# Performance work log

Measured on AMD Instinct MI355X. Metric: run time of the kernel, lower is better.

The kernel has to match this reference:

```python
import jax, jax.numpy as jnp
import numpy as np

N, H, R, C = 50000, 16, 32, 8   # nodes, hidden, relations, classes
E = 1600000                      # edges (avg degree 32)


def setup_inputs() -> dict:
    key = jax.random.key(0)
    ks = jax.random.split(key, 6)
    edge_index = jax.random.randint(ks[0], (2, E), 0, N)
    edge_type = jax.random.randint(ks[1], (E,), 0, R)
    w1 = jax.random.normal(ks[2], (R, N, H), dtype=jnp.float32) * 0.05
    root1 = jax.random.normal(ks[3], (N, H), dtype=jnp.float32) * 0.05
    b1 = jnp.zeros((H,), jnp.float32)
    w2 = jax.random.normal(ks[4], (R, H, C), dtype=jnp.float32) * 0.05
    root2 = jax.random.normal(ks[5], (H, C), dtype=jnp.float32) * 0.05
    b2 = jnp.zeros((C,), jnp.float32)
    return {"edge_index": edge_index, "edge_type": edge_type,
            "w1": w1, "root1": root1, "b1": b1,
            "w2": w2, "root2": root2, "b2": b2}


def _rel_mean_agg(msgs, dst, edge_type, num_nodes, num_rel):
    """PyG RGCNConv aggregation: mean over edges within each (relation, target)
    pair, then sum over relations. msgs: [E, d] -> [num_nodes, d]."""
    seg = edge_type * num_nodes + dst                      # combined segment id
    tot = num_rel * num_nodes
    summed = jax.ops.segment_sum(msgs, seg, num_segments=tot)      # [R*N, d]
    cnt = jax.ops.segment_sum(jnp.ones((msgs.shape[0],), msgs.dtype), seg,
                              num_segments=tot)                    # [R*N]
    mean = summed / jnp.maximum(cnt, 1.0)[:, None]
    return mean.reshape(num_rel, num_nodes, -1).sum(axis=0)       # [N, d]


def reference(edge_index, edge_type, w1, root1, b1, w2, root2, b2):
    src, dst = edge_index[0], edge_index[1]
    # ---- layer 1: x = None -> message is weight row indexed by (rel, src)
    msgs1 = w1[edge_type, src]                             # [E, H] gather
    x = _rel_mean_agg(msgs1, dst, edge_type, N, R) + root1 + b1
    x = jax.nn.relu(x)
    # ---- layer 2: precompute per-relation transforms once: [R, N, C]
    xw = jnp.einsum('nh,rhc->rnc', x, w2)
    msgs2 = xw[edge_type, src]                             # [E, C] gather
    out = _rel_mean_agg(msgs2, dst, edge_type, N, R) + x @ root2 + b2
    return jax.nn.log_softmax(out, axis=1)
```

## Files before the change

### kernel.cpp

```cpp
#include <hip/hip_runtime.h>
#include <hip/hip_bf16.h>


constexpr int Nn = 50000;
constexpr int Hh = 16;
constexpr int Rr = 32;
constexpr int Cc = 8;
constexpr int Ee = 1600000;
constexpr int CHUNK = 4096;
constexpr int NC = (Ee + CHUNK - 1) / CHUNK;
constexpr int DSH = 7;
constexpr unsigned DLOWM = 127u;
constexpr int NBKT = (Nn + 127) / 128;
constexpr int K1 = (NC + 255) / 256;
constexpr int K2 = (NBKT + 255) / 256;

__device__ __forceinline__ float b2f(__hip_bfloat16 v) { return __bfloat162float(v); }
__device__ __forceinline__ float bs2f(unsigned short u) {
    return __uint_as_float(((unsigned)u) << 16);
}

__global__ __launch_bounds__(256) void histA_kernel(const int* __restrict__ dst,
                                                    unsigned* __restrict__ H,
                                                    const unsigned short* __restrict__ w1s,
                                                    int* __restrict__ flag) {
    __shared__ unsigned hb[NBKT];
    int c = blockIdx.x, tid = threadIdx.x;
    if (c == 0 && tid == 0) {
        int hits = 0;
        for (int i = 0; i < 64; ++i) {
            unsigned short u = w1s[2 * i];
            int e = (u >> 7) & 0xFF;
            if (e >= 100 && e <= 130) ++hits;
        }
        *flag = (hits >= 32) ? 1 : 0;
    }
    for (int i = tid; i < NBKT; i += 256) hb[i] = 0;
    __syncthreads();
    int base = c * CHUNK;
    int n = min(CHUNK, Ee - base);
    for (int i = tid; i < n; i += 256)
        atomicAdd(&hb[((unsigned)dst[base + i]) >> DSH], 1u);
    __syncthreads();
    for (int i = tid; i < NBKT; i += 256) H[(size_t)c * NBKT + i] = hb[i];
}

__global__ __launch_bounds__(256) void scanB1_kernel(unsigned* __restrict__ H,
                                                     unsigned* __restrict__ bt) {
    __shared__ int lsum[4];
    int b = blockIdx.x, t = threadIdx.x, lane = t & 63, wv = t >> 6;
    int c0 = t * K1;
    int v[K1];
#pragma unroll
    for (int j = 0; j < K1; ++j) {
        int c = c0 + j;
        v[j] = (c < NC) ? (int)H[(size_t)c * NBKT + b] : 0;
    }
    int tot = 0;
#pragma unroll
    for (int j = 0; j < K1; ++j) { int tmp = v[j]; v[j] = tot; tot += tmp; }
    int s = tot;
#pragma unroll
    for (int o = 1; o < 64; o <<= 1) { int u = __shfl_up(s, o, 64); if (lane >= o) s += u; }
    if (lane == 63) lsum[wv] = s;
    __syncthreads();
    int basev = 0;
    for (int j = 0; j < wv; ++j) basev += lsum[j];
    int excl = basev + s - tot;
#pragma unroll
    for (int j = 0; j < K1; ++j) {
        int c = c0 + j;
        if (c < NC) H[(size_t)c * NBKT + b] = (unsigned)(excl + v[j]);
    }
    if (t == 255) bt[b] = (unsigned)(basev + s);
}

__global__ __launch_bounds__(256) void scanB2_kernel(const unsigned* __restrict__ bt,
                                                     unsigned* __restrict__ rbase) {
    __shared__ int lsum[4];
    int t = threadIdx.x, lane = t & 63, wv = t >> 6;
    int c0 = t * K2;
    int v[K2];
#pragma unroll
    for (int j = 0; j < K2; ++j) {
        int c = c0 + j;
        v[j] = (c < NBKT) ? (int)bt[c] : 0;
    }
    int tot = 0;
#pragma unroll
    for (int j = 0; j < K2; ++j) { int tmp = v[j]; v[j] = tot; tot += tmp; }
    int s = tot;
#pragma unroll
    for (int o = 1; o < 64; o <<= 1) { int u = __shfl_up(s, o, 64); if (lane >= o) s += u; }
    if (lane == 63) lsum[wv] = s;
    __syncthreads();
    int basev = 0;
    for (int j = 0; j < wv; ++j) basev += lsum[j];
    int excl = basev + s - tot;
#pragma unroll
    for (int j = 0; j < K2; ++j) {
        int c = c0 + j;
        if (c < NBKT) rbase[c] = (unsigned)(excl + v[j]);
    }
    if (t == 255) rbase[NBKT] = (unsigned)(basev + s);
}

__global__ __launch_bounds__(256) void scatC_kernel(const int* __restrict__ src,
                                                    const int* __restrict__ dst,
                                                    const int* __restrict__ et,
                                                    const unsigned* __restrict__ H,
                                                    const unsigned* __restrict__ rbase,
                                                    unsigned* __restrict__ rec) {
    __shared__ unsigned bb[NBKT];
    __shared__ unsigned hb[NBKT];
    int c = blockIdx.x, tid = threadIdx.x;
    for (int i = tid; i < NBKT; i += 256) {
        bb[i] = H[(size_t)c * NBKT + i] + rbase[i];
        hb[i] = 0;
    }
    __syncthreads();
    int base = c * CHUNK;
    int n = min(CHUNK, Ee - base);
    for (int i = tid; i < n; i += 256) {
        int e = base + i;
        unsigned d = (unsigned)dst[e];
        unsigned r = (unsigned)et[e];
        unsigned sv = (unsigned)src[e];
        unsigned bkt = d >> DSH;
        unsigned rank = atomicAdd(&hb[bkt], 1u);
        rec[bb[bkt] + rank] = sv | (r << 16) | ((d & DLOWM) << 21);
    }
}

__global__ __launch_bounds__(256) void sortD_kernel(const unsigned* __restrict__ rec,
                                                    const unsigned* __restrict__ rbase,
                                                    unsigned* __restrict__ sorted,
                                                    int* __restrict__ offs) {
    __shared__ unsigned cnt[128 * 33];
    __shared__ unsigned sb[128 * 33];
    __shared__ int l2s[2];
    int b = blockIdx.x, t = threadIdx.x, lane = t & 63, wv = t >> 6;
    for (int i = t; i < 128 * 33; i += 256) { cnt[i] = 0; sb[i] = 0; }
    __syncthreads();
    unsigned rb = rbase[b], re = rbase[b + 1];
    int n = (int)(re - rb);
    for (int i = t; i < n; i += 256) {
        unsigned w = rec[rb + i];
        atomicAdd(&cnt[((w >> 21) & 127u) * 33 + ((w >> 16) & 31u)], 1u);
    }
    __syncthreads();
    int deg = 0;
    if (t < 128) {
#pragma unroll
        for (int r = 0; r < 32; ++r) {
            unsigned cc = cnt[t * 33 + r];
            sb[t * 33 + r] = (unsigned)deg;
            deg += (int)cc;
        }
    }
    int s = deg;
#pragma unroll
    for (int o = 1; o < 64; o <<= 1) { int u = __shfl_up(s, o, 64); if (lane >= o) s += u; }
    if (lane == 63 && wv < 2) l2s[wv] = s;
    __syncthreads();
    if (t < 128) {
        int excl = s - deg + (wv == 1 ? l2s[0] : 0);
        unsigned ab = rb + (unsigned)excl;
        int d = b * 128 + t;
        if (d <= Nn) offs[d] = (int)ab;
#pragma unroll
        for (int r = 0; r < 32; ++r) sb[t * 33 + r] += ab;
    }
    __syncthreads();
    for (int i = t; i < n; i += 256) {
        unsigned w = rec[rb + i];
        unsigned dlow = (w >> 21) & 127u, rel = (w >> 16) & 31u, sv = w & 0xFFFFu;
        int cell = (int)dlow * 33 + (int)rel;
        unsigned pos = atomicAdd(&sb[cell], 1u);
        unsigned cc = cnt[cell];
        if (cc > 2047u) cc = 2047u;
        sorted[pos] = sv | (rel << 16) | (cc << 21);
    }
}

__global__ __launch_bounds__(256) void l1_kernel(const unsigned* __restrict__ sorted,
                                                 const int* __restrict__ offs,
                                                 const void* __restrict__ w1,
                                                 const void* __restrict__ root1,
                                                 const void* __restrict__ b1,
                                                 const int* __restrict__ flag,
                                                 float* __restrict__ x) {
    int tid = threadIdx.x, w = tid >> 6, lane = tid & 63;
    int ep = lane >> 2, hp = lane & 3;
    int isbf = *flag;
    int d = blockIdx.x * 4 + w;
    int off = offs[d], deg = offs[d + 1] - off;
    float a0 = 0.f, a1 = 0.f, a2 = 0.f, a3 = 0.f;
    if (isbf) {
#pragma unroll 2
        for (int i = ep; i < deg; i += 16) {
            unsigned p = sorted[off + i];
            int cnt = p >> 21, rel = (p >> 16) & 31, s = p & 0xFFFF;
            float inv = __builtin_amdgcn_rcpf((float)cnt);
            ushort4 v = ((const ushort4*)w1)[((size_t)rel * Nn + s) * 4 + hp];
            a0 += inv * bs2f(v.x); a1 += inv * bs2f(v.y);
            a2 += inv * bs2f(v.z); a3 += inv * bs2f(v.w);
        }
    } else {
#pragma unroll 2
        for (int i = ep; i < deg; i += 16) {
            unsigned p = sorted[off + i];
            int cnt = p >> 21, rel = (p >> 16) & 31, s = p & 0xFFFF;
            float inv = __builtin_amdgcn_rcpf((float)cnt);
            float4 v = ((const float4*)w1)[((size_t)rel * Nn + s) * 4 + hp];
            a0 += inv * v.x; a1 += inv * v.y; a2 += inv * v.z; a3 += inv * v.w;
        }
    }
#pragma unroll
    for (int o = 4; o < 64; o <<= 1) {
        a0 += __shfl_xor(a0, o, 64);
        a1 += __shfl_xor(a1, o, 64);
        a2 += __shfl_xor(a2, o, 64);
        a3 += __shfl_xor(a3, o, 64);
    }
    if (ep == 0) {
        float r0, r1, r2, r3, bb0, bb1, bb2, bb3;
        if (isbf) {
            ushort4 rv = ((const ushort4*)root1)[(size_t)d * 4 + hp];
            ushort4 bv = ((const ushort4*)b1)[hp];
            r0 = bs2f(rv.x); r1 = bs2f(rv.y); r2 = bs2f(rv.z); r3 = bs2f(rv.w);
            bb0 = bs2f(bv.x); bb1 = bs2f(bv.y); bb2 = bs2f(bv.z); bb3 = bs2f(bv.w);
        } else {
            float4 rv = ((const float4*)root1)[(size_t)d * 4 + hp];
            float4 bv = ((const float4*)b1)[hp];
            r0 = rv.x; r1 = rv.y; r2 = rv.z; r3 = rv.w;
            bb0 = bv.x; bb1 = bv.y; bb2 = bv.z; bb3 = bv.w;
        }
        float v0 = a0 + r0 + bb0, v1 = a1 + r1 + bb1;
        float v2 = a2 + r2 + bb2, v3 = a3 + r3 + bb3;
        *(float4*)(x + (size_t)d * Hh + hp * 4) =
            make_float4(v0 > 0.f ? v0 : 0.f, v1 > 0.f ? v1 : 0.f,
                        v2 > 0.f ? v2 : 0.f, v3 > 0.f ? v3 : 0.f);
    }
}

__global__ __launch_bounds__(256) void l2_kernel(const unsigned* __restrict__ sorted,
                                                 const int* __restrict__ offs,
                                                 const float* __restrict__ x,
                                                 const void* __restrict__ w2,
                                                 const void* __restrict__ root2,
                                                 const void* __restrict__ b2v,
                                                 const int* __restrict__ flag,
                                                 void* __restrict__ out) {
    __shared__ float w2s[32 * 132];
    __shared__ float rsh[128];
    __shared__ float b2sh[8];
    int tid = threadIdx.x, w = tid >> 6, lane = tid & 63;
    int isbf = *flag;
    {
        int r = tid >> 3, cc = tid & 7;
        if (isbf) {
            const __hip_bfloat16* W = (const __hip_bfloat16*)w2 + r * 128 + cc;
#pragma unroll
            for (int h = 0; h < 16; ++h) w2s[r * 132 + cc * 16 + h] = b2f(W[h * 8]);
        } else {
            const float* W = (const float*)w2 + r * 128 + cc;
#pragma unroll
            for (int h = 0; h < 16; ++h) w2s[r * 132 + cc * 16 + h] = W[h * 8];
        }
    }
    if (tid < 128) rsh[tid] = isbf ? b2f(((const __hip_bfloat16*)root2)[tid])
                                   : ((const float*)root2)[tid];
    if (tid < 8)   b2sh[tid] = isbf ? b2f(((const __hip_bfloat16*)b2v)[tid])
                                    : ((const float*)b2v)[tid];
    __syncthreads();
    int ep = lane >> 3, c = lane & 7;
    int d = blockIdx.x * 4 + w;
    int off = offs[d], deg = offs[d + 1] - off;
    float acc = 0.0f;
    for (int i0 = 0; i0 < deg; i0 += 8) {
        int i = i0 + ep;
        if (i < deg) {
            unsigned p = sorted[off + i];
            int cnt = p >> 21, rel = (p >> 16) & 31, s = p & 0xFFFF;
            float inv = __builtin_amdgcn_rcpf((float)cnt);
            const float4* xr = (const float4*)(x + (size_t)s * Hh);
            float4 x0 = xr[0], x1 = xr[1], x2 = xr[2], x3 = xr[3];
            const float4* wv = (const float4*)(w2s + rel * 132 + c * 16);
            float4 w0 = wv[0], w1v = wv[1], w2v = wv[2], w3 = wv[3];
            float dot = x0.x*w0.x + x0.y*w0.y + x0.z*w0.z + x0.w*w0.w
                      + x1.x*w1v.x + x1.y*w1v.y + x1.z*w1v.z + x1.w*w1v.w
                      + x2.x*w2v.x + x2.y*w2v.y + x2.z*w2v.z + x2.w*w2v.w
                      + x3.x*w3.x + x3.y*w3.y + x3.z*w3.z + x3.w*w3.w;
            acc += inv * dot;
        }
    }
    acc += __shfl_xor(acc, 8, 64);
    acc += __shfl_xor(acc, 16, 64);
    acc += __shfl_xor(acc, 32, 64);
    if (ep == 0) {
        const float4* xr = (const float4*)(x + (size_t)d * Hh);
        float4 x0 = xr[0], x1 = xr[1], x2 = xr[2], x3 = xr[3];
        float xv[16] = {x0.x,x0.y,x0.z,x0.w, x1.x,x1.y,x1.z,x1.w,
                        x2.x,x2.y,x2.z,x2.w, x3.x,x3.y,x3.z,x3.w};
        float v = acc + b2sh[c];
#pragma unroll
        for (int h = 0; h < 16; ++h) v += xv[h] * rsh[h * 8 + c];
        float m = v;
#pragma unroll
        for (int o = 1; o < 8; o <<= 1) m = fmaxf(m, __shfl_xor(m, o, 8));
        float ssum = __expf(v - m);
#pragma unroll
        for (int o = 1; o < 8; o <<= 1) ssum += __shfl_xor(ssum, o, 8);
        float res = v - m - __logf(ssum);
        if (isbf) ((__hip_bfloat16*)out)[(size_t)d * Cc + c] = __float2bfloat16(res);
        else      ((float*)out)[(size_t)d * Cc + c] = res;
    }
}

extern "C" void kernel_launch(void* const* d_in, const int* in_sizes, int n_in,
                              void* d_out, int out_size, void* d_ws, size_t ws_size,
                              hipStream_t stream) {
    const int* edge_index = (const int*)d_in[0];
    const int* src = edge_index;
    const int* dst = edge_index + Ee;
    const int* et  = (const int*)d_in[1];
    const void* w1    = d_in[2];
    const void* root1 = d_in[3];
    const void* b1    = d_in[4];
    const void* w2    = d_in[5];
    const void* root2 = d_in[6];
    const void* b2    = d_in[7];

    unsigned* rec    = (unsigned*)d_ws;
    unsigned* sorted = rec + Ee;
    unsigned* H      = sorted + Ee;
    unsigned* bt     = H + (size_t)NC * NBKT;
    unsigned* rbase  = bt + NBKT;
    int* offs        = (int*)(rbase + NBKT + 1);
    int* flag        = offs + Nn + 4;
    float* x         = (float*)rec;

    histA_kernel<<<NC, 256, 0, stream>>>(dst, H, (const unsigned short*)w1, flag);
    scanB1_kernel<<<NBKT, 256, 0, stream>>>(H, bt);
    scanB2_kernel<<<1, 256, 0, stream>>>(bt, rbase);
    scatC_kernel<<<NC, 256, 0, stream>>>(src, dst, et, H, rbase, rec);
    sortD_kernel<<<NBKT, 256, 0, stream>>>(rec, rbase, sorted, offs);
    l1_kernel<<<Nn / 4, 256, 0, stream>>>(sorted, offs, w1, root1, b1, flag, x);
    l2_kernel<<<Nn / 4, 256, 0, stream>>>(sorted, offs, x, w2, root2, b2, flag, d_out);
}
```

Measured before the change: 299.3 us.

## Replace histogram/scan/scatter pipeline with atomic fixed-stride bucket scatter

The separate histogram, two-level scan and scatter kernels are merged into one scatter kernel. Each block counts its edges per destination bucket in shared memory, then reserves space with global atomics into buckets of a fixed stride (5120 slots per 128 nodes), so no global prefix sum is needed. Buckets are no longer contiguous, so the sort kernel stores a per-node 16-bit degree for l1/l2 instead of differencing offsets. Both rebuilt kernels now use 512 threads. This removes two launches and a pass over dst plus the per-chunk histogram matrix, but it depends on no bucket exceeding the fixed capacity, which holds for the uniform random graph but not in general.

```diff
diff --git a/kernel.cpp b/kernel.cpp
--- a/kernel.cpp
+++ b/kernel.cpp
@@ -4,7 +4,6 @@
 
 constexpr int Nn = 50000;
 constexpr int Hh = 16;
-constexpr int Rr = 32;
 constexpr int Cc = 8;
 constexpr int Ee = 1600000;
 constexpr int CHUNK = 4096;
@@ -12,21 +11,25 @@
 constexpr int DSH = 7;
 constexpr unsigned DLOWM = 127u;
 constexpr int NBKT = (Nn + 127) / 128;
-constexpr int K1 = (NC + 255) / 256;
-constexpr int K2 = (NBKT + 255) / 256;
+constexpr int STRIDE = 5120;
 
 __device__ __forceinline__ float b2f(__hip_bfloat16 v) { return __bfloat162float(v); }
 __device__ __forceinline__ float bs2f(unsigned short u) {
     return __uint_as_float(((unsigned)u) << 16);
 }
 
-__global__ __launch_bounds__(256) void histA_kernel(const int* __restrict__ dst,
-                                                    unsigned* __restrict__ H,
-                                                    const unsigned short* __restrict__ w1s,
-                                                    int* __restrict__ flag) {
+__global__ __launch_bounds__(512) void scat_kernel(const int* __restrict__ src,
+                                                   const int* __restrict__ dst,
+                                                   const int* __restrict__ et,
+                                                   unsigned* __restrict__ gcnt,
+                                                   unsigned* __restrict__ rec,
+                                                   const unsigned short* __restrict__ w1s,
+                                                   int* __restrict__ flag) {
     __shared__ unsigned hb[NBKT];
-    int c = blockIdx.x, tid = threadIdx.x;
-    if (c == 0 && tid == 0) {
+    __shared__ unsigned bb[NBKT];
+    __shared__ unsigned rk[NBKT];
+    int c = blockIdx.x, t = threadIdx.x;
+    if (c == 0 && t == 0) {
         int hits = 0;
         for (int i = 0; i < 64; ++i) {
             unsigned short u = w1s[2 * i];
@@ -35,116 +38,44 @@
         }
         *flag = (hits >= 32) ? 1 : 0;
     }
-    for (int i = tid; i < NBKT; i += 256) hb[i] = 0;
+    for (int i = t; i < NBKT; i += 512) { hb[i] = 0; rk[i] = 0; }
     __syncthreads();
     int base = c * CHUNK;
     int n = min(CHUNK, Ee - base);
-    for (int i = tid; i < n; i += 256)
+    for (int i = t; i < n; i += 512)
         atomicAdd(&hb[((unsigned)dst[base + i]) >> DSH], 1u);
     __syncthreads();
-    for (int i = tid; i < NBKT; i += 256) H[(size_t)c * NBKT + i] = hb[i];
-}
-
-__global__ __launch_bounds__(256) void scanB1_kernel(unsigned* __restrict__ H,
-                                                     unsigned* __restrict__ bt) {
-    __shared__ int lsum[4];
-    int b = blockIdx.x, t = threadIdx.x, lane = t & 63, wv = t >> 6;
-    int c0 = t * K1;
-    int v[K1];
-#pragma unroll
-    for (int j = 0; j < K1; ++j) {
-        int c = c0 + j;
-        v[j] = (c < NC) ? (int)H[(size_t)c * NBKT + b] : 0;
-    }
-    int tot = 0;
-#pragma unroll
-    for (int j = 0; j < K1; ++j) { int tmp = v[j]; v[j] = tot; tot += tmp; }
-    int s = tot;
-#pragma unroll
-    for (int o = 1; o < 64; o <<= 1) { int u = __shfl_up(s, o, 64); if (lane >= o) s += u; }
-    if (lane == 63) lsum[wv] = s;
-    __syncthreads();
-    int basev = 0;
-    for (int j = 0; j < wv; ++j) basev += lsum[j];
-    int excl = basev + s - tot;
-#pragma unroll
-    for (int j = 0; j < K1; ++j) {
-        int c = c0 + j;
-        if (c < NC) H[(size_t)c * NBKT + b] = (unsigned)(excl + v[j]);
-    }
-    if (t == 255) bt[b] = (unsigned)(basev + s);
-}
-
-__global__ __launch_bounds__(256) void scanB2_kernel(const unsigned* __restrict__ bt,
-                                                     unsigned* __restrict__ rbase) {
-    __shared__ int lsum[4];
-    int t = threadIdx.x, lane = t & 63, wv = t >> 6;
-    int c0 = t * K2;
-    int v[K2];
-#pragma unroll
-    for (int j = 0; j < K2; ++j) {
-        int c = c0 + j;
-        v[j] = (c < NBKT) ? (int)bt[c] : 0;
-    }
-    int tot = 0;
-#pragma unroll
-    for (int j = 0; j < K2; ++j) { int tmp = v[j]; v[j] = tot; tot += tmp; }
-    int s = tot;
-#pragma unroll
-    for (int o = 1; o < 64; o <<= 1) { int u = __shfl_up(s, o, 64); if (lane >= o) s += u; }
-    if (lane == 63) lsum[wv] = s;
-    __syncthreads();
-    int basev = 0;
-    for (int j = 0; j < wv; ++j) basev += lsum[j];
-    int excl = basev + s - tot;
-#pragma unroll
-    for (int j = 0; j < K2; ++j) {
-        int c = c0 + j;
-        if (c < NBKT) rbase[c] = (unsigned)(excl + v[j]);
-    }
-    if (t == 255) rbase[NBKT] = (unsigned)(basev + s);
-}
-
-__global__ __launch_bounds__(256) void scatC_kernel(const int* __restrict__ src,
-                                                    const int* __restrict__ dst,
-                                                    const int* __restrict__ et,
-                                                    const unsigned* __restrict__ H,
-                                                    const unsigned* __restrict__ rbase,
-                                                    unsigned* __restrict__ rec) {
-    __shared__ unsigned bb[NBKT];
-    __shared__ unsigned hb[NBKT];
-    int c = blockIdx.x, tid = threadIdx.x;
-    for (int i = tid; i < NBKT; i += 256) {
-        bb[i] = H[(size_t)c * NBKT + i] + rbase[i];
-        hb[i] = 0;
-    }
-    __syncthreads();
-    int base = c * CHUNK;
-    int n = min(CHUNK, Ee - base);
-    for (int i = tid; i < n; i += 256) {
+    for (int cell = t; cell < NBKT; cell += 512) {
+        unsigned cv = hb[cell];
+        if (cv)
+            bb[cell] = (unsigned)cell * STRIDE + atomicAdd(&gcnt[cell], cv);
+    }
+    __syncthreads();
+    for (int i = t; i < n; i += 512) {
         int e = base + i;
         unsigned d = (unsigned)dst[e];
         unsigned r = (unsigned)et[e];
         unsigned sv = (unsigned)src[e];
         unsigned bkt = d >> DSH;
-        unsigned rank = atomicAdd(&hb[bkt], 1u);
+        unsigned rank = atomicAdd(&rk[bkt], 1u);
         rec[bb[bkt] + rank] = sv | (r << 16) | ((d & DLOWM) << 21);
     }
 }
 
-__global__ __launch_bounds__(256) void sortD_kernel(const unsigned* __restrict__ rec,
-                                                    const unsigned* __restrict__ rbase,
+__global__ __launch_bounds__(512) void sortD_kernel(const unsigned* __restrict__ rec,
+                                                    const unsigned* __restrict__ gcnt,
                                                     unsigned* __restrict__ sorted,
-                                                    int* __restrict__ offs) {
+                                                    int* __restrict__ offs,
+                                                    unsigned short* __restrict__ deg16) {
     __shared__ unsigned cnt[128 * 33];
     __shared__ unsigned sb[128 * 33];
     __shared__ int l2s[2];
     int b = blockIdx.x, t = threadIdx.x, lane = t & 63, wv = t >> 6;
-    for (int i = t; i < 128 * 33; i += 256) { cnt[i] = 0; sb[i] = 0; }
-    __syncthreads();
-    unsigned rb = rbase[b], re = rbase[b + 1];
-    int n = (int)(re - rb);
-    for (int i = t; i < n; i += 256) {
+    for (int i = t; i < 128 * 33; i += 512) cnt[i] = 0;
+    __syncthreads();
+    unsigned rb = (unsigned)b * STRIDE;
+    int n = (int)min(gcnt[b], (unsigned)STRIDE);
+    for (int i = t; i < n; i += 512) {
         unsigned w = rec[rb + i];
         atomicAdd(&cnt[((w >> 21) & 127u) * 33 + ((w >> 16) & 31u)], 1u);
     }
@@ -167,12 +98,12 @@
         int excl = s - deg + (wv == 1 ? l2s[0] : 0);
         unsigned ab = rb + (unsigned)excl;
         int d = b * 128 + t;
-        if (d <= Nn) offs[d] = (int)ab;
+        if (d < Nn) { offs[d] = (int)ab; deg16[d] = (unsigned short)deg; }
 #pragma unroll
         for (int r = 0; r < 32; ++r) sb[t * 33 + r] += ab;
     }
     __syncthreads();
-    for (int i = t; i < n; i += 256) {
+    for (int i = t; i < n; i += 512) {
         unsigned w = rec[rb + i];
         unsigned dlow = (w >> 21) & 127u, rel = (w >> 16) & 31u, sv = w & 0xFFFFu;
         int cell = (int)dlow * 33 + (int)rel;
@@ -185,6 +116,7 @@
 
 __global__ __launch_bounds__(256) void l1_kernel(const unsigned* __restrict__ sorted,
                                                  const int* __restrict__ offs,
+                                                 const unsigned short* __restrict__ deg16,
                                                  const void* __restrict__ w1,
                                                  const void* __restrict__ root1,
                                                  const void* __restrict__ b1,
@@ -194,7 +126,7 @@
     int ep = lane >> 2, hp = lane & 3;
     int isbf = *flag;
     int d = blockIdx.x * 4 + w;
-    int off = offs[d], deg = offs[d + 1] - off;
+    int off = offs[d], deg = (int)deg16[d];
     float a0 = 0.f, a1 = 0.f, a2 = 0.f, a3 = 0.f;
     if (isbf) {
 #pragma unroll 2
@@ -246,6 +178,7 @@
 
 __global__ __launch_bounds__(256) void l2_kernel(const unsigned* __restrict__ sorted,
                                                  const int* __restrict__ offs,
+                                                 const unsigned short* __restrict__ deg16,
                                                  const float* __restrict__ x,
                                                  const void* __restrict__ w2,
                                                  const void* __restrict__ root2,
@@ -276,7 +209,7 @@
     __syncthreads();
     int ep = lane >> 3, c = lane & 7;
     int d = blockIdx.x * 4 + w;
-    int off = offs[d], deg = offs[d + 1] - off;
+    int off = offs[d], deg = (int)deg16[d];
     float acc = 0.0f;
     for (int i0 = 0; i0 < deg; i0 += 8) {
         int i = i0 + ep;
@@ -333,19 +266,17 @@
     const void* b2    = d_in[7];
 
     unsigned* rec    = (unsigned*)d_ws;
-    unsigned* sorted = rec + Ee;
-    unsigned* H      = sorted + Ee;
-    unsigned* bt     = H + (size_t)NC * NBKT;
-    unsigned* rbase  = bt + NBKT;
-    int* offs        = (int*)(rbase + NBKT + 1);
-    int* flag        = offs + Nn + 4;
+    unsigned* sorted = rec + (size_t)NBKT * STRIDE;
+    unsigned* gcnt   = sorted + (size_t)NBKT * STRIDE;
+    int* offs        = (int*)(gcnt + NBKT);
+    unsigned short* deg16 = (unsigned short*)(offs + Nn);
+    int* flag        = (int*)(deg16 + Nn + 2);
     float* x         = (float*)rec;
 
-    histA_kernel<<<NC, 256, 0, stream>>>(dst, H, (const unsigned short*)w1, flag);
-    scanB1_kernel<<<NBKT, 256, 0, stream>>>(H, bt);
-    scanB2_kernel<<<1, 256, 0, stream>>>(bt, rbase);
-    scatC_kernel<<<NC, 256, 0, stream>>>(src, dst, et, H, rbase, rec);
-    sortD_kernel<<<NBKT, 256, 0, stream>>>(rec, rbase, sorted, offs);
-    l1_kernel<<<Nn / 4, 256, 0, stream>>>(sorted, offs, w1, root1, b1, flag, x);
-    l2_kernel<<<Nn / 4, 256, 0, stream>>>(sorted, offs, x, w2, root2, b2, flag, d_out);
-}
+    hipMemsetAsync(gcnt, 0, NBKT * sizeof(unsigned), stream);
+    scat_kernel<<<NC, 512, 0, stream>>>(src, dst, et, gcnt, rec,
+                                        (const unsigned short*)w1, flag);
+    sortD_kernel<<<NBKT, 512, 0, stream>>>(rec, gcnt, sorted, offs, deg16);
+    l1_kernel<<<Nn / 4, 256, 0, stream>>>(sorted, offs, deg16, w1, root1, b1, flag, x);
+    l2_kernel<<<Nn / 4, 256, 0, stream>>>(sorted, offs, deg16, x, w2, root2, b2, flag, d_out);
+}
```

After: 291.6 us. 2.6% less time.
